# Performance work log

Measured on AMD Instinct MI355X. Metric: run time of the kernel, lower is better.

## Reference

```python
import jax, jax.numpy as jnp
import numpy as np

DIM = 768
NUM_HEADS = 12
HEAD_DIM = DIM // NUM_HEADS
BASE = 10000.0


def rotate_half(x):
    x1, x2 = jnp.split(x, 2, axis=-1)
    return jnp.concatenate((-x2, x1), axis=-1)


def rope_cos_sin(seq_len, dim, dtype):
    inv_freq = 1.0 / (BASE ** (jnp.arange(0, dim, 2, dtype=jnp.float32) / dim))
    t = jnp.arange(seq_len, dtype=jnp.float32)
    freqs = jnp.einsum('i,j->ij', t, inv_freq)  # [N, dim/2]
    emb = jnp.concatenate((freqs, freqs), axis=-1)  # [N, dim]
    return jnp.cos(emb).astype(dtype), jnp.sin(emb).astype(dtype)


def setup_inputs() -> dict:
    key = jax.random.key(0)
    k1, k2, k3, k4 = jax.random.split(key, 4)
    B, N, C = 1, 4096, DIM
    x = jax.random.normal(k1, (B, N, C), dtype=jnp.float32)
    s = 1.0 / np.sqrt(C)
    qkv_w = jax.random.normal(k2, (3 * C, C), dtype=jnp.float32) * s
    proj_w = jax.random.normal(k3, (C, C), dtype=jnp.float32) * s
    proj_b = jax.random.normal(k4, (C,), dtype=jnp.float32) * 0.01
    return {"x": x, "qkv_w": qkv_w, "proj_w": proj_w, "proj_b": proj_b}


def reference(x, qkv_w, proj_w, proj_b):
    B, N, C = x.shape
    H, D = NUM_HEADS, HEAD_DIM
    scale = D ** -0.5
    qkv = jnp.einsum('bnc,oc->bno', x, qkv_w)           # [B, N, 3C]
    qkv = qkv.reshape(B, N, 3, H, D).transpose(2, 0, 3, 1, 4)  # [3, B, H, N, D]
    q, k, v = qkv[0], qkv[1], qkv[2]
    cos, sin = rope_cos_sin(N, D, x.dtype)              # [N, D] each
    cos = cos[None, None]                               # [1,1,N,D]
    sin = sin[None, None]
    q = q * cos + rotate_half(q) * sin
    k = k * cos + rotate_half(k) * sin
    attn = jnp.einsum('bhqd,bhkd->bhqk', q, k) * scale  # [B,H,N,N]
    attn = jax.nn.softmax(attn, axis=-1)
    out = jnp.einsum('bhqk,bhkd->bhqd', attn, v)        # [B,H,N,D]
    out = out.transpose(0, 2, 1, 3).reshape(B, N, C)
    return jnp.einsum('bnc,oc->bno', out, proj_w) + proj_b
```

## Files before the change

### kernel.cpp

```cpp
#include <hip/hip_runtime.h>
#include <hip/hip_bf16.h>
#include <math.h>

#define DIM 768
#define NHEADS 12
#define HD 64
#define SEQ 4096
#define KSPLIT 2

typedef __bf16 bf16x8 __attribute__((ext_vector_type(8)));
typedef float f32x4 __attribute__((ext_vector_type(4)));

__device__ inline ushort f2bf(float f) {
    __bf16 b = (__bf16)f;
    union { __bf16 b; ushort u; } v; v.b = b;
    return v.u;
}

__device__ inline ushort f2bf_tw(float f) {
    union { float f; uint u; } v; v.f = f;
    uint r = v.u + 0x7FFF + ((v.u >> 16) & 1);
    return (ushort)(r >> 16);
}

__device__ inline void gload16(const ushort* gsrc, ushort* lbase) {
    __builtin_amdgcn_global_load_lds(
        (const __attribute__((address_space(1))) uint*)gsrc,
        (__attribute__((address_space(3))) uint*)lbase, 16, 0, 0);
}

__global__ __launch_bounds__(256)
void prep(const float* __restrict__ x, const float* __restrict__ qkv_w,
          const float* __restrict__ proj_w,
          ushort* __restrict__ xb, ushort* __restrict__ qwb,
          ushort* __restrict__ pwb, float2* __restrict__ tab)
{
    const int b = blockIdx.x;
    if (b < 5376) {
        const float* src; ushort* dst; int i;
        if (b < 3072)      { src = x;      dst = xb;  i = b * 256 + threadIdx.x; }
        else if (b < 4800) { src = qkv_w;  dst = qwb; i = (b - 3072) * 256 + threadIdx.x; }
        else               { src = proj_w; dst = pwb; i = (b - 4800) * 256 + threadIdx.x; }
        const float4 v = ((const float4*)src)[i];
        ushort4 w;
        w.x = f2bf(v.x); w.y = f2bf(v.y); w.z = f2bf(v.z); w.w = f2bf(v.w);
        ((ushort4*)dst)[i] = w;
    } else {
        const int idx = (b - 5376) * 256 + threadIdx.x;
        const int j = idx & 31;
        const int n = idx >> 5;
        const float invf = (float)pow(10000.0, -(double)j / 32.0);
        const float ang  = (float)n * invf;
        double s, c;
        sincos((double)ang, &s, &c);
        tab[idx] = make_float2((float)c, (float)s);
    }
}

__global__ __launch_bounds__(256)
void gemm_qkv(const ushort* __restrict__ A, const ushort* __restrict__ B,
              const float2* __restrict__ tab,
              ushort* __restrict__ Qb, ushort* __restrict__ Kb,
              ushort* __restrict__ Vp)
{
    constexpr int BM = 128, BN = 128, BK = 64;
    __shared__ __attribute__((aligned(16))) ushort Ah[2][BM][BK];
    __shared__ __attribute__((aligned(16))) ushort Bh[2][BN][BK];

    const int t    = threadIdx.x;
    const int lane = t & 63;
    const int wv   = t >> 6;
    const int wm   = (wv >> 1) * 64;
    const int wn   = (wv & 1) * 64;
    const int m0   = blockIdx.y * BM;
    const int n0   = blockIdx.x * BN;

    f32x4 acc[4][4] = {};

    const int lrow = lane >> 3;
    const int lch  = (lane & 7) * 8;

    #pragma unroll
    for (int i = 0; i < 4; ++i) {
        const int rb = i * 32 + wv * 8;
        gload16(&A[(size_t)(m0 + rb + lrow) * DIM + lch], &Ah[0][rb][0]);
        gload16(&B[(size_t)(n0 + rb + lrow) * DIM + lch], &Bh[0][rb][0]);
    }
    __syncthreads();

    int cur = 0;
    for (int k0 = 0; k0 < DIM; k0 += BK) {
        if (k0 + BK < DIM) {
            #pragma unroll
            for (int i = 0; i < 4; ++i) {
                const int rb = i * 32 + wv * 8;
                gload16(&A[(size_t)(m0 + rb + lrow) * DIM + k0 + BK + lch],
                        &Ah[cur ^ 1][rb][0]);
                gload16(&B[(size_t)(n0 + rb + lrow) * DIM + k0 + BK + lch],
                        &Bh[cur ^ 1][rb][0]);
            }
        }

        #pragma unroll
        for (int ks = 0; ks < BK; ks += 32) {
            const int koff = ks + ((lane >> 4) << 3);
            const int rs = lane & 15;
            bf16x8 af[4], bf[4];
            #pragma unroll
            for (int i = 0; i < 4; ++i) {
                af[i] = *(const bf16x8*)&Ah[cur][wm + i * 16 + rs][koff];
                bf[i] = *(const bf16x8*)&Bh[cur][wn + i * 16 + rs][koff];
            }
            #pragma unroll
            for (int i = 0; i < 4; ++i)
                #pragma unroll
                for (int j = 0; j < 4; ++j)
                    acc[i][j] = __builtin_amdgcn_mfma_f32_16x16x32_bf16(
                        af[i], bf[j], acc[i][j], 0, 0, 0);
        }
        __syncthreads();
        cur ^= 1;
    }

    const int rsel  = lane & 15;
    const int quad  = lane >> 4;
    const int rbase = m0 + wm + (quad << 2);
    const int c0    = n0 + wn;
    const int tt    = c0 / DIM;
    const int h     = (c0 % DIM) >> 6;

    if (tt == 2) {
        const int T = (m0 + wm) >> 6;
        #pragma unroll
        for (int j = 0; j < 4; ++j) {
            const int d = rsel + 16 * j;
            ushort vv[16];
            #pragma unroll
            for (int r = 0; r < 4; ++r)
                #pragma unroll
                for (int i = 0; i < 4; ++i)
                    vv[4 * r + i] = f2bf(acc[i][j][r]);
            ushort* dst = &Vp[((size_t)h * HD + d) * SEQ + T * 64 + 16 * quad];
            *(float4*)&dst[0] = *(const float4*)&vv[0];
            *(float4*)&dst[8] = *(const float4*)&vv[8];
        }
    } else {
        ushort* dstb = (tt == 0 ? Qb : Kb) + (size_t)h * SEQ * HD;
        const float qs = (tt == 0) ? 0.18033688011112042f : 1.0f;
        #pragma unroll
        for (int i = 0; i < 4; ++i)
            #pragma unroll
            for (int r = 0; r < 4; ++r) {
                const int n = rbase + i * 16 + r;
                #pragma unroll
                for (int j = 0; j < 2; ++j) {
                    const float a = acc[i][j][r];
                    const float b = acc[i][j + 2][r];
                    const float2 cs2 = tab[n * 32 + rsel + 16 * j];
                    dstb[(size_t)n * HD + rsel + 16 * j]      = f2bf((a * cs2.x - b * cs2.y) * qs);
                    dstb[(size_t)n * HD + rsel + 16 * j + 32] = f2bf((b * cs2.x + a * cs2.y) * qs);
                }
            }
    }
}

__global__ __launch_bounds__(256, 3)
void flash_mfma(const ushort* __restrict__ Qb, const ushort* __restrict__ Kb,
                const ushort* __restrict__ Vp,
                float* __restrict__ Opart, float* __restrict__ lpart)
{
    __shared__ ushort Ks[2][64][68];
    __shared__ ushort Vs[2][64][68];
    __shared__ ushort Pl[4][32][68];

    const int t    = threadIdx.x;
    const int lane = t & 63;
    const int wv   = t >> 6;
    const int rsel = lane & 15;
    const int quad = lane >> 4;

    const int p  = blockIdx.x + 32 * (blockIdx.y + 12 * blockIdx.z);
    const int c  = p & 7;
    const int r  = p >> 3;
    const int gi = r >> 5;
    const int xq = r & 31;
    const int g  = gi * 8 + c;
    const int h    = g % 12;
    const int part = g / 12;

    const int q0   = xq * 128 + wv * 32;
    const int Tbeg = (part * (SEQ / KSPLIT)) >> 6;
    const int Tend = Tbeg + (SEQ / KSPLIT) / 64;

    const int crow = t >> 2;
    const int ccol = (t & 3) * 16;

    bf16x8 aq[2][2];
    #pragma unroll
    for (int mi = 0; mi < 2; ++mi)
        #pragma unroll
        for (int ks = 0; ks < 2; ++ks)
            aq[mi][ks] = *(const bf16x8*)&Qb[((size_t)h * SEQ + q0 + 16 * mi + rsel) * HD
                                             + ks * 32 + quad * 8];

    f32x4 accO[2][4] = {};
    float lsum[2][4] = {};

    {
        const ushort* ksrc = &Kb[((size_t)h * SEQ + Tbeg * 64 + crow) * HD + ccol];
        const float4 k0 = *(const float4*)&ksrc[0];
        const float4 k1 = *(const float4*)&ksrc[8];
        const ushort* vsrc = &Vp[((size_t)h * HD + crow) * SEQ + Tbeg * 64 + ccol];
        const float4 v0 = *(const float4*)&vsrc[0];
        const float4 v1 = *(const float4*)&vsrc[8];
        *(float4*)&Ks[0][crow][ccol]     = k0;
        *(float4*)&Ks[0][crow][ccol + 8] = k1;
        *(float4*)&Vs[0][crow][ccol]     = v0;
        *(float4*)&Vs[0][crow][ccol + 8] = v1;
    }
    __syncthreads();

    int cur = 0;
    for (int T = Tbeg; T < Tend; ++T) {
        const int Tn = (T + 1 < Tend) ? T + 1 : T;
        const ushort* ksrc = &Kb[((size_t)h * SEQ + Tn * 64 + crow) * HD + ccol];
        const float4 kn0 = *(const float4*)&ksrc[0];
        const float4 kn1 = *(const float4*)&ksrc[8];
        const ushort* vsrc = &Vp[((size_t)h * HD + crow) * SEQ + Tn * 64 + ccol];
        const float4 vn0 = *(const float4*)&vsrc[0];
        const float4 vn1 = *(const float4*)&vsrc[8];

        bf16x8 bk[4][2], bv[4][2];
        #pragma unroll
        for (int n = 0; n < 4; ++n)
            #pragma unroll
            for (int ks = 0; ks < 2; ++ks) {
                bk[n][ks] = *(const bf16x8*)&Ks[cur][16 * n + rsel][32 * ks + quad * 8];
                bv[n][ks] = *(const bf16x8*)&Vs[cur][16 * n + rsel][32 * ks + quad * 8];
            }

        #pragma unroll
        for (int mi = 0; mi < 2; ++mi) {
            f32x4 accS[4] = {};
            #pragma unroll
            for (int ks = 0; ks < 2; ++ks)
                #pragma unroll
                for (int n = 0; n < 4; ++n)
                    accS[n] = __builtin_amdgcn_mfma_f32_16x16x32_bf16(
                        aq[mi][ks], bk[n][ks], accS[n], 0, 0, 0);

            #pragma unroll
            for (int r = 0; r < 4; ++r) {
                const float p0 = __builtin_amdgcn_exp2f(accS[0][r]);
                const float p1 = __builtin_amdgcn_exp2f(accS[1][r]);
                const float p2 = __builtin_amdgcn_exp2f(accS[2][r]);
                const float p3 = __builtin_amdgcn_exp2f(accS[3][r]);
                ushort4 pw;
                pw.x = f2bf_tw(p0); pw.y = f2bf_tw(p1);
                pw.z = f2bf_tw(p2); pw.w = f2bf_tw(p3);
                *(ushort4*)&Pl[wv][16 * mi + 4 * quad + r][4 * rsel] = pw;
                lsum[mi][r] += (p0 + p1) + (p2 + p3);
            }
        }

        asm volatile("s_waitcnt lgkmcnt(0)" ::: "memory");

        #pragma unroll
        for (int mi = 0; mi < 2; ++mi) {
            bf16x8 ap[2];
            ap[0] = *(const bf16x8*)&Pl[wv][16 * mi + rsel][quad * 8];
            ap[1] = *(const bf16x8*)&Pl[wv][16 * mi + rsel][32 + quad * 8];
            #pragma unroll
            for (int ks = 0; ks < 2; ++ks)
                #pragma unroll
                for (int j = 0; j < 4; ++j)
                    accO[mi][j] = __builtin_amdgcn_mfma_f32_16x16x32_bf16(
                        ap[ks], bv[j][ks], accO[mi][j], 0, 0, 0);
        }

        *(float4*)&Ks[cur ^ 1][crow][ccol]     = kn0;
        *(float4*)&Ks[cur ^ 1][crow][ccol + 8] = kn1;
        *(float4*)&Vs[cur ^ 1][crow][ccol]     = vn0;
        *(float4*)&Vs[cur ^ 1][crow][ccol + 8] = vn1;
        __syncthreads();
        cur ^= 1;
    }

    #pragma unroll
    for (int mi = 0; mi < 2; ++mi)
        #pragma unroll
        for (int r = 0; r < 4; ++r) {
            float s = lsum[mi][r];
            s += __shfl_xor(s, 1);
            s += __shfl_xor(s, 2);
            s += __shfl_xor(s, 4);
            s += __shfl_xor(s, 8);
            lsum[mi][r] = s;
        }

    float* Ob = Opart + ((size_t)part * NHEADS + h) * SEQ * HD;
    float* lb = lpart + ((size_t)part * NHEADS + h) * SEQ;
    #pragma unroll
    for (int mi = 0; mi < 2; ++mi)
        #pragma unroll
        for (int r = 0; r < 4; ++r) {
            const int n = q0 + 16 * mi + 4 * quad + r;
            #pragma unroll
            for (int j = 0; j < 4; ++j)
                Ob[(size_t)n * HD + 16 * j + rsel] = accO[mi][j][r];
            if (rsel == 0) lb[n] = lsum[mi][r];
        }
}

__global__ __launch_bounds__(256)
void merge_k(const float* __restrict__ Opart, const float* __restrict__ lpart,
             ushort* __restrict__ AO)
{
    const int idx = blockIdx.x * 256 + threadIdx.x;
    const int dg = idx & 15;
    const int n  = (idx >> 4) & (SEQ - 1);
    const int h  = idx >> 16;

    float4 o = make_float4(0.f, 0.f, 0.f, 0.f);
    float l = 0.f;
    #pragma unroll
    for (int p = 0; p < KSPLIT; ++p) {
        const float4 v = *(const float4*)&Opart[(((size_t)p * NHEADS + h) * SEQ + n) * HD + dg * 4];
        o.x += v.x; o.y += v.y; o.z += v.z; o.w += v.w;
        l += lpart[((size_t)p * NHEADS + h) * SEQ + n];
    }
    const float inv = 1.f / l;
    ushort4 w;
    w.x = f2bf(o.x * inv); w.y = f2bf(o.y * inv);
    w.z = f2bf(o.z * inv); w.w = f2bf(o.w * inv);
    *(ushort4*)&AO[(size_t)n * DIM + h * HD + dg * 4] = w;
}

__global__ __launch_bounds__(256)
void gemm_proj(const ushort* __restrict__ A, const ushort* __restrict__ B,
               const float* __restrict__ bias, float* __restrict__ out)
{
    constexpr int BM = 128, BN = 128, BK = 64;
    __shared__ __attribute__((aligned(16))) ushort As[2][BM][BK];
    __shared__ __attribute__((aligned(16))) ushort Bs[2][BN][BK];

    const int t    = threadIdx.x;
    const int lane = t & 63;
    const int wv   = t >> 6;
    const int wm   = (wv >> 1) * 64;
    const int wn   = (wv & 1) * 64;
    const int m0   = blockIdx.y * BM;
    const int n0   = blockIdx.x * BN;

    f32x4 acc[4][4] = {};

    const int lrow = lane >> 3;
    const int lch  = (lane & 7) * 8;

    #pragma unroll
    for (int i = 0; i < 4; ++i) {
        const int rb = i * 32 + wv * 8;
        gload16(&A[(size_t)(m0 + rb + lrow) * DIM + lch], &As[0][rb][0]);
        gload16(&B[(size_t)(n0 + rb + lrow) * DIM + lch], &Bs[0][rb][0]);
    }
    __syncthreads();

    int cur = 0;
    for (int k0 = 0; k0 < DIM; k0 += BK) {
        if (k0 + BK < DIM) {
            #pragma unroll
            for (int i = 0; i < 4; ++i) {
                const int rb = i * 32 + wv * 8;
                gload16(&A[(size_t)(m0 + rb + lrow) * DIM + k0 + BK + lch],
                        &As[cur ^ 1][rb][0]);
                gload16(&B[(size_t)(n0 + rb + lrow) * DIM + k0 + BK + lch],
                        &Bs[cur ^ 1][rb][0]);
            }
        }

        #pragma unroll
        for (int ks = 0; ks < BK; ks += 32) {
            const int koff = ks + ((lane >> 4) << 3);
            const int rs = lane & 15;
            bf16x8 af[4], bf[4];
            #pragma unroll
            for (int i = 0; i < 4; ++i) {
                af[i] = *(const bf16x8*)&As[cur][wm + i * 16 + rs][koff];
                bf[i] = *(const bf16x8*)&Bs[cur][wn + i * 16 + rs][koff];
            }
            #pragma unroll
            for (int i = 0; i < 4; ++i)
                #pragma unroll
                for (int j = 0; j < 4; ++j)
                    acc[i][j] = __builtin_amdgcn_mfma_f32_16x16x32_bf16(
                        af[i], bf[j], acc[i][j], 0, 0, 0);
        }
        __syncthreads();
        cur ^= 1;
    }

    const int rbase = m0 + wm + ((lane >> 4) << 2);
    const int cbase = n0 + wn + (lane & 15);

    #pragma unroll
    for (int j = 0; j < 4; ++j) {
        const int col = cbase + j * 16;
        const float bv = bias[col];
        #pragma unroll
        for (int i = 0; i < 4; ++i) {
            const int row0 = rbase + i * 16;
            #pragma unroll
            for (int r = 0; r < 4; ++r)
                out[(size_t)(row0 + r) * DIM + col] = acc[i][j][r] + bv;
        }
    }
}

extern "C" void kernel_launch(void* const* d_in, const int* in_sizes, int n_in,
                              void* d_out, int out_size, void* d_ws, size_t ws_size,
                              hipStream_t stream)
{
    const float* x      = (const float*)d_in[0];
    const float* qkv_w  = (const float*)d_in[1];
    const float* proj_w = (const float*)d_in[2];
    const float* proj_b = (const float*)d_in[3];

    const size_t headsz = (size_t)NHEADS * SEQ * HD;
    char* p = (char*)d_ws;
    ushort* Qb    = (ushort*)p;                 p += headsz * 2;
    ushort* Kb    = (ushort*)p;                 p += headsz * 2;
    ushort* Vp    = (ushort*)p;                 p += headsz * 2;
    ushort* AO    = (ushort*)p;                 p += (size_t)SEQ * DIM * 2;
    float*  Opart = (float*)p;                  p += (size_t)KSPLIT * headsz * 4;
    float*  lpart = (float*)p;                  p += (size_t)KSPLIT * NHEADS * SEQ * 4;
    float2* tab   = (float2*)p;                 p += (size_t)SEQ * 32 * sizeof(float2);
    ushort* xb    = (ushort*)p;                 p += (size_t)SEQ * DIM * 2;
    ushort* qwb   = (ushort*)p;                 p += (size_t)3 * DIM * DIM * 2;
    ushort* pwb   = (ushort*)p;
    float*  out   = (float*)d_out;

    prep<<<5888, 256, 0, stream>>>(x, qkv_w, proj_w, xb, qwb, pwb, tab);

    gemm_qkv<<<dim3(3 * DIM / 128, SEQ / 128), 256, 0, stream>>>(
        xb, qwb, tab, Qb, Kb, Vp);

    flash_mfma<<<dim3(SEQ / 128, NHEADS, KSPLIT), 256, 0, stream>>>(
        Qb, Kb, Vp, Opart, lpart);

    merge_k<<<(NHEADS * SEQ * 16) / 256, 256, 0, stream>>>(Opart, lpart, AO);

    gemm_proj<<<dim3(DIM / 128, SEQ / 128), 256, 0, stream>>>(
        AO, pwb, proj_b, out);
}
```

Baseline: 202.4 us.

## Compute S transposed so P stays in registers, dropping the LDS round-trip

```diff
diff --git a/kernel.cpp b/kernel.cpp
--- a/kernel.cpp
+++ b/kernel.cpp
@@ -134,15 +134,17 @@
         #pragma unroll
         for (int j = 0; j < 4; ++j) {
             const int d = rsel + 16 * j;
-            ushort vv[16];
-            #pragma unroll
-            for (int r = 0; r < 4; ++r)
+            ushort vvA[8], vvB[8];
+            #pragma unroll
+            for (int i2 = 0; i2 < 2; ++i2)
                 #pragma unroll
-                for (int i = 0; i < 4; ++i)
-                    vv[4 * r + i] = f2bf(acc[i][j][r]);
-            ushort* dst = &Vp[((size_t)h * HD + d) * SEQ + T * 64 + 16 * quad];
-            *(float4*)&dst[0] = *(const float4*)&vv[0];
-            *(float4*)&dst[8] = *(const float4*)&vv[8];
+                for (int r = 0; r < 4; ++r) {
+                    vvA[4 * i2 + r] = f2bf(acc[i2][j][r]);
+                    vvB[4 * i2 + r] = f2bf(acc[2 + i2][j][r]);
+                }
+            ushort* dst = &Vp[((size_t)h * HD + d) * SEQ + T * 64];
+            *(float4*)&dst[8 * quad]      = *(const float4*)&vvA[0];
+            *(float4*)&dst[32 + 8 * quad] = *(const float4*)&vvB[0];
         }
     } else {
         ushort* dstb = (tt == 0 ? Qb : Kb) + (size_t)h * SEQ * HD;
@@ -171,7 +173,6 @@
 {
     __shared__ ushort Ks[2][64][68];
     __shared__ ushort Vs[2][64][68];
-    __shared__ ushort Pl[4][32][68];
 
     const int t    = threadIdx.x;
     const int lane = t & 63;
@@ -204,7 +205,7 @@
                                              + ks * 32 + quad * 8];
 
     f32x4 accO[2][4] = {};
-    float lsum[2][4] = {};
+    float lsum[2] = {0.f, 0.f};
 
     {
         const ushort* ksrc = &Kb[((size_t)h * SEQ + Tbeg * 64 + crow) * HD + ccol];
@@ -242,40 +243,40 @@
         #pragma unroll
         for (int mi = 0; mi < 2; ++mi) {
             f32x4 accS[4] = {};
+            __builtin_amdgcn_s_setprio(1);
             #pragma unroll
             for (int ks = 0; ks < 2; ++ks)
                 #pragma unroll
                 for (int n = 0; n < 4; ++n)
                     accS[n] = __builtin_amdgcn_mfma_f32_16x16x32_bf16(
-                        aq[mi][ks], bk[n][ks], accS[n], 0, 0, 0);
-
+                        bk[n][ks], aq[mi][ks], accS[n], 0, 0, 0);
+            __builtin_amdgcn_s_setprio(0);
+
+            union { ushort u[8]; bf16x8 v; } ap0, ap1;
+            float ls = 0.f;
             #pragma unroll
             for (int r = 0; r < 4; ++r) {
                 const float p0 = __builtin_amdgcn_exp2f(accS[0][r]);
                 const float p1 = __builtin_amdgcn_exp2f(accS[1][r]);
                 const float p2 = __builtin_amdgcn_exp2f(accS[2][r]);
                 const float p3 = __builtin_amdgcn_exp2f(accS[3][r]);
-                ushort4 pw;
-                pw.x = f2bf_tw(p0); pw.y = f2bf_tw(p1);
-                pw.z = f2bf_tw(p2); pw.w = f2bf_tw(p3);
-                *(ushort4*)&Pl[wv][16 * mi + 4 * quad + r][4 * rsel] = pw;
-                lsum[mi][r] += (p0 + p1) + (p2 + p3);
-            }
-        }
-
-        asm volatile("s_waitcnt lgkmcnt(0)" ::: "memory");
-
-        #pragma unroll
-        for (int mi = 0; mi < 2; ++mi) {
-            bf16x8 ap[2];
-            ap[0] = *(const bf16x8*)&Pl[wv][16 * mi + rsel][quad * 8];
-            ap[1] = *(const bf16x8*)&Pl[wv][16 * mi + rsel][32 + quad * 8];
-            #pragma unroll
-            for (int ks = 0; ks < 2; ++ks)
-                #pragma unroll
-                for (int j = 0; j < 4; ++j)
-                    accO[mi][j] = __builtin_amdgcn_mfma_f32_16x16x32_bf16(
-                        ap[ks], bv[j][ks], accO[mi][j], 0, 0, 0);
+                ap0.u[r]     = f2bf_tw(p0);
+                ap0.u[4 + r] = f2bf_tw(p1);
+                ap1.u[r]     = f2bf_tw(p2);
+                ap1.u[4 + r] = f2bf_tw(p3);
+                ls += (p0 + p1) + (p2 + p3);
+            }
+            lsum[mi] += ls;
+
+            __builtin_amdgcn_s_setprio(1);
+            #pragma unroll
+            for (int j = 0; j < 4; ++j) {
+                accO[mi][j] = __builtin_amdgcn_mfma_f32_16x16x32_bf16(
+                    ap0.v, bv[j][0], accO[mi][j], 0, 0, 0);
+                accO[mi][j] = __builtin_amdgcn_mfma_f32_16x16x32_bf16(
+                    ap1.v, bv[j][1], accO[mi][j], 0, 0, 0);
+            }
+            __builtin_amdgcn_s_setprio(0);
         }
 
         *(float4*)&Ks[cur ^ 1][crow][ccol]     = kn0;
@@ -287,29 +288,26 @@
     }
 
     #pragma unroll
-    for (int mi = 0; mi < 2; ++mi)
-        #pragma unroll
-        for (int r = 0; r < 4; ++r) {
-            float s = lsum[mi][r];
-            s += __shfl_xor(s, 1);
-            s += __shfl_xor(s, 2);
-            s += __shfl_xor(s, 4);
-            s += __shfl_xor(s, 8);
-            lsum[mi][r] = s;
-        }
+    for (int mi = 0; mi < 2; ++mi) {
+        float s = lsum[mi];
+        s += __shfl_xor(s, 16);
+        s += __shfl_xor(s, 32);
+        lsum[mi] = s;
+    }
 
     float* Ob = Opart + ((size_t)part * NHEADS + h) * SEQ * HD;
     float* lb = lpart + ((size_t)part * NHEADS + h) * SEQ;
     #pragma unroll
-    for (int mi = 0; mi < 2; ++mi)
+    for (int mi = 0; mi < 2; ++mi) {
         #pragma unroll
         for (int r = 0; r < 4; ++r) {
             const int n = q0 + 16 * mi + 4 * quad + r;
             #pragma unroll
             for (int j = 0; j < 4; ++j)
                 Ob[(size_t)n * HD + 16 * j + rsel] = accO[mi][j][r];
-            if (rsel == 0) lb[n] = lsum[mi][r];
-        }
+        }
+        if (quad == 0) lb[q0 + 16 * mi + rsel] = lsum[mi];
+    }
 }
 
 __global__ __launch_bounds__(256)
```

Result: slower. 237.8 us (+17.5%).
